# Kernel tuning notes

Measured on AMD Instinct MI355X. Metric: run time of the kernel, lower is better.

## Reference

```python
import jax, jax.numpy as jnp
import numpy as np

N, E, B = 10000, 20000, 400
ND, ED, D = 32, 16, 64


def setup_inputs() -> dict:
    key = jax.random.key(0)
    ks = jax.random.split(key, 32)

    def lin(k, out_d, in_d):
        kw, kb = jax.random.split(k)
        s = 1.0 / np.sqrt(in_d)
        return (jax.random.uniform(kw, (out_d, in_d), jnp.float32, -s, s),
                jax.random.uniform(kb, (out_d,), jnp.float32, -s, s))

    W_in, b_in = lin(ks[0], D, ND)
    W_e1, b_e1 = lin(ks[1], D, ED)
    W_e2, b_e2 = lin(ks[2], D * D, D)
    b_conv = jax.random.uniform(ks[3], (D,), jnp.float32, -1/8.0, 1/8.0)
    W_ih, b_ih = lin(ks[4], 3 * D, D)
    W_hh, b_hh = lin(ks[5], 3 * D, D)
    W_ih_l, b_ih_l = lin(ks[6], 4 * D, 2 * D)
    W_hh_l, b_hh_l = lin(ks[7], 4 * D, D)
    W_o1, b_o1 = lin(ks[8], D, 2 * D)
    W_o2, b_o2 = lin(ks[9], 1, D)

    x = jax.random.normal(ks[10], (N, ND), jnp.float32)
    edge_attr = jax.random.normal(ks[11], (E, ED), jnp.float32)
    edge_index = jax.random.randint(ks[12], (2, E), 0, N, jnp.int64)
    batch = jnp.sort(jax.random.randint(ks[13], (N,), 0, B, jnp.int64))

    return dict(x=x, edge_attr=edge_attr,
                W_in=W_in, b_in=b_in, W_e1=W_e1, b_e1=b_e1, W_e2=W_e2, b_e2=b_e2,
                b_conv=b_conv, W_ih=W_ih, b_ih=b_ih, W_hh=W_hh, b_hh=b_hh,
                W_ih_l=W_ih_l, b_ih_l=b_ih_l, W_hh_l=W_hh_l, b_hh_l=b_hh_l,
                W_o1=W_o1, b_o1=b_o1, W_o2=W_o2, b_o2=b_o2,
                edge_index=edge_index, batch=batch)


def reference(x, edge_attr, W_in, b_in, W_e1, b_e1, W_e2, b_e2, b_conv,
              W_ih, b_ih, W_hh, b_hh, W_ih_l, b_ih_l, W_hh_l, b_hh_l,
              W_o1, b_o1, W_o2, b_o2, edge_index, batch):
    src, dst = edge_index[0], edge_index[1]

    # in_linear
    out = jax.nn.relu(x @ W_in.T + b_in)            # [N, D]
    h = out                                          # GRU hidden (layer=1, seq=1)

    # edge-conditioned weights: MLP(edge_attr) -> [E, D, D]
    ew = (jax.nn.relu(edge_attr @ W_e1.T + b_e1) @ W_e2.T + b_e2).reshape(E, D, D)
    cnt = jnp.maximum(jax.ops.segment_sum(jnp.ones((E,), x.dtype), dst, N), 1.0)

    for _ in range(3):
        # NNConv: gather src nodes, per-edge matmul, scatter-mean to dst, + bias
        msg = jnp.einsum('ed,edf->ef', out[src], ew)                 # [E, D]
        agg = jax.ops.segment_sum(msg, dst, N) / cnt[:, None] + b_conv
        m = jax.nn.relu(agg)
        # GRU cell (torch gate order r, z, n)
        gi = m @ W_ih.T + b_ih
        gh = h @ W_hh.T + b_hh
        i_r, i_z, i_n = jnp.split(gi, 3, axis=-1)
        h_r, h_z, h_n = jnp.split(gh, 3, axis=-1)
        r = jax.nn.sigmoid(i_r + h_r)
        z = jax.nn.sigmoid(i_z + h_z)
        n = jnp.tanh(i_n + r * h_n)
        h = (1.0 - z) * n + z * h
        out = h

    # Set2Set pooling, processing_steps=3
    q_star = jnp.zeros((B, 2 * D), x.dtype)
    hl = jnp.zeros((B, D), x.dtype)
    cl = jnp.zeros((B, D), x.dtype)
    for _ in range(3):
        g = q_star @ W_ih_l.T + b_ih_l + hl @ W_hh_l.T + b_hh_l
        gi_, gf_, gg_, go_ = jnp.split(g, 4, axis=-1)   # torch order i,f,g,o
        cl = jax.nn.sigmoid(gf_) * cl + jax.nn.sigmoid(gi_) * jnp.tanh(gg_)
        hl = jax.nn.sigmoid(go_) * jnp.tanh(cl)
        q = hl                                           # [B, D]
        e = jnp.sum(out * q[batch], axis=-1)             # [N]
        mmax = jax.ops.segment_max(e, batch, B)
        a = jnp.exp(e - mmax[batch])
        a = a / jax.ops.segment_sum(a, batch, B)[batch]
        r_ = jax.ops.segment_sum(a[:, None] * out, batch, B)  # [B, D]
        q_star = jnp.concatenate([q, r_], axis=-1)

    o = jax.nn.relu(q_star @ W_o1.T + b_o1) @ W_o2.T + b_o2
    return o.reshape(-1)
```

## Files before the change

### kernel.cpp

```cpp
#include <hip/hip_runtime.h>
#include <math.h>


#define Nn 10000
#define Ee 20000
#define Bb 400
#define KSTEPS 130
#define S2S_CHUNK 1024

typedef __attribute__((ext_vector_type(8))) short bf16x8_t;
typedef __attribute__((ext_vector_type(4))) float f32x4_t;

__device__ __forceinline__ float sigmoidf_(float x) { return 1.f / (1.f + expf(-x)); }

__device__ __forceinline__ void split8(const float* p, bf16x8_t& Ahi_, bf16x8_t& Alo_) {
    union { bf16x8_t v; unsigned u[4]; } hi, lo;
#pragma unroll
    for (int ii = 0; ii < 4; ++ii) {
        float pa = p[2 * ii], pb = p[2 * ii + 1];
        unsigned ua = __float_as_uint(pa), ub = __float_as_uint(pb);
        hi.u[ii] = (ua >> 16) | (ub & 0xFFFF0000u);
        float la = pa - __uint_as_float(ua & 0xFFFF0000u);
        float lb = pb - __uint_as_float(ub & 0xFFFF0000u);
        lo.u[ii] = (__float_as_uint(la) >> 16) | (__float_as_uint(lb) & 0xFFFF0000u);
    }
    Ahi_ = hi.v; Alo_ = lo.v;
}

__global__ __launch_bounds__(256) void k_in_linear(const float* __restrict__ x,
                                                   const float* __restrict__ Win,
                                                   const float* __restrict__ bin,
                                                   float* __restrict__ out) {
    int idx = blockIdx.x * 256 + threadIdx.x;
    if (idx >= Nn * 64) return;
    int n = idx >> 6, j = idx & 63;
    const float* xr = x + n * 32;
    const float* w = Win + j * 32;
    float acc = bin[j];
#pragma unroll
    for (int k = 0; k < 32; ++k) acc += xr[k] * w[k];
    out[idx] = fmaxf(acc, 0.f);
}

__global__ __launch_bounds__(256) void k_edge_mlp1(const float* __restrict__ ea,
                                                   const float* __restrict__ W1,
                                                   const float* __restrict__ b1,
                                                   float* __restrict__ eh) {
    int idx = blockIdx.x * 256 + threadIdx.x;
    if (idx >= Ee * 64) return;
    int e = idx >> 6, j = idx & 63;
    const float* ar = ea + e * 16;
    const float* w = W1 + j * 16;
    float acc = b1[j];
#pragma unroll
    for (int k = 0; k < 16; ++k) acc += ar[k] * w[k];
    eh[idx] = fmaxf(acc, 0.f);
}

__global__ __launch_bounds__(256) void k_make_Bfat(const float* __restrict__ W2,
                                                   const float* __restrict__ b2,
                                                   unsigned short* __restrict__ Bfat) {
    int idx = blockIdx.x * 256 + threadIdx.x;
    if (idx >= KSTEPS * 4096) return;
    int i  = idx & 7;
    int l  = (idx >> 3) & 63;
    int nq = (idx >> 9) & 3;
    int h  = (idx >> 11) & 1;
    int ks = idx >> 12;
    int kap = ks * 32 + (l >> 4) * 8 + i;
    int f = nq * 16 + (l & 15);
    float w;
    if (kap < 4096) {
        int q = kap >> 6, d = kap & 63;
        w = W2[(size_t)(d * 64 + f) * 64 + q];
    } else {
        int d = kap - 4096;
        w = b2[d * 64 + f];
    }
    unsigned u = __float_as_uint(w);
    unsigned short outv;
    if (h == 0) {
        outv = (unsigned short)(u >> 16);
    } else {
        float lo = w - __uint_as_float(u & 0xFFFF0000u);
        outv = (unsigned short)(__float_as_uint(lo) >> 16);
    }
    Bfat[idx] = outv;
}

__global__ __launch_bounds__(256) void k_make_Wg(const float* __restrict__ Wih,
                                                 const float* __restrict__ Whh,
                                                 unsigned short* __restrict__ Wg) {
    int idx = blockIdx.x * 256 + threadIdx.x;
    if (idx >= 4 * 2 * 16 * 64 * 8) return;
    int i  = idx & 7;
    int l  = (idx >> 3) & 63;
    int t  = (idx >> 9) & 15;
    int h  = (idx >> 13) & 1;
    int ks = idx >> 14;
    int k = ks * 32 + (l >> 4) * 8 + i;
    int u = t * 16 + (l & 15);
    int j = u & 63, part = u >> 6;
    float w = 0.f;
    if (part == 0) w = (k < 64) ? Wih[(size_t)j * 64 + k]          : Whh[(size_t)j * 64 + (k - 64)];
    if (part == 1) w = (k < 64) ? Wih[(size_t)(64 + j) * 64 + k]   : Whh[(size_t)(64 + j) * 64 + (k - 64)];
    if (part == 2) w = (k < 64) ? Wih[(size_t)(128 + j) * 64 + k]  : 0.f;
    if (part == 3) w = (k < 64) ? 0.f : Whh[(size_t)(128 + j) * 64 + (k - 64)];
    unsigned uu = __float_as_uint(w);
    unsigned short outv;
    if (h == 0) {
        outv = (unsigned short)(uu >> 16);
    } else {
        float lo = w - __uint_as_float(uu & 0xFFFF0000u);
        outv = (unsigned short)(__float_as_uint(lo) >> 16);
    }
    Wg[idx] = outv;
}

__global__ __launch_bounds__(256, 3) void k_msg_mfma(const float* __restrict__ out,
                                                     const float* __restrict__ eh,
                                                     const unsigned short* __restrict__ Bfat,
                                                     const int* __restrict__ ei,
                                                     float* __restrict__ agg) {
    __shared__ float outs[128][64];
    __shared__ float ehs[128][20];
    __shared__ unsigned short Bst[4096];
    int tid = threadIdx.x;
    int ebase = blockIdx.x * 128;
    int ksplit = blockIdx.y;

    int ks0 = ksplit * 32 + (ksplit < 2 ? ksplit : 2);
    int ks1 = ks0 + (ksplit < 2 ? 33 : 32);
    int q0 = ks0 >> 1;
    int qn = ((min(ks1, 128) - 1) >> 1) - q0 + 1;

#pragma unroll
    for (int pass = 0; pass < 2; ++pass) {
        int el = pass * 64 + (tid >> 2), seg = tid & 3;
        int eg = ebase + el;
        bool v = eg < Ee;
        int s = v ? ei[eg] : 0;
        const float* orow = out + (size_t)s * 64 + seg * 16;
        float4 z = make_float4(0.f, 0.f, 0.f, 0.f);
#pragma unroll
        for (int c = 0; c < 4; ++c) {
            float4 ov = v ? *(const float4*)(orow + c * 4) : z;
            int f = (seg * 4 + c) ^ (el & 7);
            *(float4*)&outs[el][f * 4] = ov;
        }
        const float* erow = eh + (size_t)eg * 64;
        for (int j = seg; j < qn; j += 4)
            ehs[el][j] = v ? erow[q0 + j] : 0.f;
    }

    const float4* bsrc = (const float4*)(Bfat + (size_t)ks0 * 4096);
    float4 bpre0 = bsrc[tid];
    float4 bpre1 = bsrc[256 + tid];

    int lane = tid & 63;
    int wtile = tid >> 6;
    int m16 = lane & 15;
    int g = lane >> 4;
    int erA = wtile * 32 + m16;
    int erB = erA + 16;
    int eswA = erA & 7;
    int eswB = erB & 7;

    f32x4_t acc[2][4];
#pragma unroll
    for (int t = 0; t < 2; ++t)
#pragma unroll
        for (int nq = 0; nq < 4; ++nq) acc[t][nq] = (f32x4_t){0.f, 0.f, 0.f, 0.f};

    for (int ks = ks0; ks < ks1; ++ks) {
        *(float4*)&Bst[(size_t)tid * 8] = bpre0;
        *(float4*)&Bst[2048 + (size_t)tid * 8] = bpre1;
        __syncthreads();

        if (ks + 1 < ks1) {
            const float4* bn = (const float4*)(Bfat + (size_t)(ks + 1) * 4096);
            bpre0 = bn[tid];
            bpre1 = bn[256 + tid];
        }

        bf16x8_t bhi[4], blo[4];
#pragma unroll
        for (int nq = 0; nq < 4; ++nq) {
            bhi[nq] = *(const bf16x8_t*)&Bst[((size_t)nq * 64 + lane) * 8];
            blo[nq] = *(const bf16x8_t*)&Bst[((size_t)(4 + nq) * 64 + lane) * 8];
        }

        int fbase = (ks < 128) ? (ks & 1) * 8 + g * 2 : (ks - 128) * 8 + g * 2;

        {
            float ehq = (ks < 128) ? ehs[erA][(ks >> 1) - q0] : 1.f;
            float4 o1 = *(const float4*)&outs[erA][(fbase ^ eswA) * 4];
            float4 o2 = *(const float4*)&outs[erA][((fbase + 1) ^ eswA) * 4];
            float p[8] = {o1.x * ehq, o1.y * ehq, o1.z * ehq, o1.w * ehq,
                          o2.x * ehq, o2.y * ehq, o2.z * ehq, o2.w * ehq};
            bf16x8_t Ahi, Alo;
            split8(p, Ahi, Alo);
#pragma unroll
            for (int nq = 0; nq < 4; ++nq) {
                acc[0][nq] = __builtin_amdgcn_mfma_f32_16x16x32_bf16(Ahi, bhi[nq], acc[0][nq], 0, 0, 0);
                acc[0][nq] = __builtin_amdgcn_mfma_f32_16x16x32_bf16(Ahi, blo[nq], acc[0][nq], 0, 0, 0);
                acc[0][nq] = __builtin_amdgcn_mfma_f32_16x16x32_bf16(Alo, bhi[nq], acc[0][nq], 0, 0, 0);
            }
        }
        {
            float ehq = (ks < 128) ? ehs[erB][(ks >> 1) - q0] : 1.f;
            float4 o1 = *(const float4*)&outs[erB][(fbase ^ eswB) * 4];
            float4 o2 = *(const float4*)&outs[erB][((fbase + 1) ^ eswB) * 4];
            float p[8] = {o1.x * ehq, o1.y * ehq, o1.z * ehq, o1.w * ehq,
                          o2.x * ehq, o2.y * ehq, o2.z * ehq, o2.w * ehq};
            bf16x8_t Ahi, Alo;
            split8(p, Ahi, Alo);
#pragma unroll
            for (int nq = 0; nq < 4; ++nq) {
                acc[1][nq] = __builtin_amdgcn_mfma_f32_16x16x32_bf16(Ahi, bhi[nq], acc[1][nq], 0, 0, 0);
                acc[1][nq] = __builtin_amdgcn_mfma_f32_16x16x32_bf16(Ahi, blo[nq], acc[1][nq], 0, 0, 0);
                acc[1][nq] = __builtin_amdgcn_mfma_f32_16x16x32_bf16(Alo, bhi[nq], acc[1][nq], 0, 0, 0);
            }
        }
        __syncthreads();
    }

#pragma unroll
    for (int t = 0; t < 2; ++t) {
#pragma unroll
        for (int r = 0; r < 4; ++r) {
            int el = wtile * 32 + t * 16 + g * 4 + r;
            int eg = ebase + el;
            if (eg >= Ee) continue;
            int dn = ei[Ee + eg];
#pragma unroll
            for (int nq = 0; nq < 4; ++nq)
                atomicAdd(&agg[(size_t)dn * 64 + nq * 16 + m16], acc[t][nq][r]);
        }
    }
}

__global__ __launch_bounds__(256) void k_gru_mfma(const float* __restrict__ agg,
                                                  const float* __restrict__ cnt,
                                                  const float* __restrict__ bconv,
                                                  const unsigned short* __restrict__ Wg,
                                                  const float* __restrict__ bih,
                                                  const float* __restrict__ bhh,
                                                  float* __restrict__ out) {
    __shared__ float ms[64][68];
    __shared__ float hs[64][68];
    int tid = threadIdx.x;
    int nbase = blockIdx.x * 64;

    {
        int nl = tid >> 2, seg = tid & 3;
        int ng = nbase + nl;
        bool v = ng < Nn;
        float c = v ? cnt[ng] : 1.f;
        c = c < 1.f ? 1.f : c;
        float rc = 1.f / c;
        const float* arow = agg + (size_t)ng * 64 + seg * 16;
        const float* hrow = out + (size_t)ng * 64 + seg * 16;
#pragma unroll
        for (int c4 = 0; c4 < 4; ++c4) {
            int col = seg * 16 + c4 * 4;
            float4 z = make_float4(0.f, 0.f, 0.f, 0.f);
            float4 av = v ? *(const float4*)(arow + c4 * 4) : z;
            float4 hv = v ? *(const float4*)(hrow + c4 * 4) : z;
            ms[nl][col + 0] = fmaxf(av.x * rc + bconv[col + 0], 0.f);
            ms[nl][col + 1] = fmaxf(av.y * rc + bconv[col + 1], 0.f);
            ms[nl][col + 2] = fmaxf(av.z * rc + bconv[col + 2], 0.f);
            ms[nl][col + 3] = fmaxf(av.w * rc + bconv[col + 3], 0.f);
            *(float4*)&hs[nl][col] = hv;
        }
    }
    __syncthreads();

    int lane = tid & 63;
    int wtile = tid >> 6;
    int m16 = lane & 15;
    int g = lane >> 4;
    int er = wtile * 16 + m16;

    f32x4_t acc[16];
#pragma unroll
    for (int t = 0; t < 16; ++t) acc[t] = (f32x4_t){0.f, 0.f, 0.f, 0.f};

#pragma unroll
    for (int ks = 0; ks < 4; ++ks) {
        const float* src = (ks < 2) ? &ms[er][ks * 32 + g * 8]
                                    : &hs[er][(ks - 2) * 32 + g * 8];
        float p[8];
#pragma unroll
        for (int ii = 0; ii < 8; ++ii) p[ii] = src[ii];
        bf16x8_t Ahi, Alo;
        split8(p, Ahi, Alo);
        const unsigned short* bstep = Wg + (size_t)ks * (2 * 16 * 512);
#pragma unroll
        for (int t = 0; t < 16; ++t) {
            bf16x8_t bhi = *(const bf16x8_t*)(bstep + ((size_t)t * 64 + lane) * 8);
            bf16x8_t blo = *(const bf16x8_t*)(bstep + ((size_t)(16 + t) * 64 + lane) * 8);
            acc[t] = __builtin_amdgcn_mfma_f32_16x16x32_bf16(Ahi, bhi, acc[t], 0, 0, 0);
            acc[t] = __builtin_amdgcn_mfma_f32_16x16x32_bf16(Ahi, blo, acc[t], 0, 0, 0);
            acc[t] = __builtin_amdgcn_mfma_f32_16x16x32_bf16(Alo, bhi, acc[t], 0, 0, 0);
        }
    }

#pragma unroll
    for (int t2 = 0; t2 < 4; ++t2) {
        int jj = t2 * 16 + m16;
        float br = bih[jj] + bhh[jj];
        float bz = bih[64 + jj] + bhh[64 + jj];
        float bin_ = bih[128 + jj];
        float bhn = bhh[128 + jj];
#pragma unroll
        for (int r = 0; r < 4; ++r) {
            int nl2 = wtile * 16 + g * 4 + r;
            int ng2 = nbase + nl2;
            if (ng2 >= Nn) continue;
            float rg = sigmoidf_(acc[t2][r] + br);
            float z  = sigmoidf_(acc[4 + t2][r] + bz);
            float nn = tanhf(acc[8 + t2][r] + bin_ + rg * (acc[12 + t2][r] + bhn));
            float hv = hs[nl2][jj];
            out[(size_t)ng2 * 64 + jj] = (1.f - z) * nn + z * hv;
        }
    }
}

__global__ __launch_bounds__(256) void k_count_deg(const int* __restrict__ ei,
                                                   float* __restrict__ cnt) {
    int e = blockIdx.x * 256 + threadIdx.x;
    if (e >= Ee) return;
    atomicAdd(&cnt[ei[Ee + e]], 1.f);
}

__global__ __launch_bounds__(256) void k_count_batch(const int* __restrict__ batch,
                                                     int* __restrict__ bcount) {
    int n = blockIdx.x * 256 + threadIdx.x;
    if (n >= Nn) return;
    atomicAdd(&bcount[batch[n]], 1);
}

__global__ __launch_bounds__(64) void k_scan_batch(const int* __restrict__ bcount,
                                                   int* __restrict__ bstart) {
    int lane = threadIdx.x;
    const int PER = (Bb + 63) / 64;
    int base = lane * PER;
    int v[PER];
    int s = 0;
#pragma unroll
    for (int i = 0; i < PER; ++i) {
        int idx = base + i;
        int c = (idx < Bb) ? bcount[idx] : 0;
        v[i] = s;
        s += c;
    }
    int inc = s;
#pragma unroll
    for (int o = 1; o < 64; o <<= 1) {
        int t = __shfl_up(inc, o, 64);
        if (lane >= o) inc += t;
    }
    int excl = inc - s;
    int total = __shfl(inc, 63, 64);
#pragma unroll
    for (int i = 0; i < PER; ++i) {
        int idx = base + i;
        if (idx < Bb) bstart[idx] = excl + v[i];
    }
    if (lane == 63) bstart[Bb] = total;
}

__device__ __forceinline__ float block_reduce_max_(float v, float* red, int tid) {
#pragma unroll
    for (int o = 32; o; o >>= 1) v = fmaxf(v, __shfl_xor(v, o, 64));
    if ((tid & 63) == 0) red[tid >> 6] = v;
    __syncthreads();
    float r = fmaxf(fmaxf(red[0], red[1]), fmaxf(red[2], red[3]));
    __syncthreads();
    return r;
}
__device__ __forceinline__ float block_reduce_sum_(float v, float* red, int tid) {
#pragma unroll
    for (int o = 32; o; o >>= 1) v += __shfl_xor(v, o, 64);
    if ((tid & 63) == 0) red[tid >> 6] = v;
    __syncthreads();
    float r = (red[0] + red[1]) + (red[2] + red[3]);
    __syncthreads();
    return r;
}

__global__ __launch_bounds__(256) void k_set2set(const float* __restrict__ out,
                                                 const int* __restrict__ bstart,
                                                 const float* __restrict__ Wil,
                                                 const float* __restrict__ bil,
                                                 const float* __restrict__ Whl,
                                                 const float* __restrict__ bhl,
                                                 const float* __restrict__ Wo1,
                                                 const float* __restrict__ bo1,
                                                 const float* __restrict__ Wo2,
                                                 const float* __restrict__ bo2,
                                                 float* __restrict__ outp) {
    __shared__ float qs[128];
    __shared__ float hs2[64];
    __shared__ float cs[64];
    __shared__ float g_lds[256];
    __shared__ float e_lds[S2S_CHUNK];
    __shared__ float red[4];
    __shared__ float rpart[4][64];

    int b = blockIdx.x, tid = threadIdx.x;
    int lane = tid & 63, wv = tid >> 6;
    int s = bstart[b], eend = bstart[b + 1];
    int cntb = eend - s;

    if (tid < 128) qs[tid] = 0.f;
    if (tid < 64) { hs2[tid] = 0.f; cs[tid] = 0.f; }
    __syncthreads();

    for (int step = 0; step < 3; ++step) {
        {
            int u = tid;
            float acc = bil[u] + bhl[u];
            const float4* wi = (const float4*)(Wil + (size_t)u * 128);
#pragma unroll
            for (int k4 = 0; k4 < 32; ++k4) {
                float4 w = wi[k4];
                acc += qs[k4 * 4 + 0] * w.x + qs[k4 * 4 + 1] * w.y +
                       qs[k4 * 4 + 2] * w.z + qs[k4 * 4 + 3] * w.w;
            }
            const float4* wh = (const float4*)(Whl + (size_t)u * 64);
#pragma unroll
            for (int k4 = 0; k4 < 16; ++k4) {
                float4 w = wh[k4];
                acc += hs2[k4 * 4 + 0] * w.x + hs2[k4 * 4 + 1] * w.y +
                       hs2[k4 * 4 + 2] * w.z + hs2[k4 * 4 + 3] * w.w;
            }
            g_lds[u] = acc;
        }
        __syncthreads();
        if (tid < 64) {
            float c = sigmoidf_(g_lds[64 + tid]) * cs[tid] +
                      sigmoidf_(g_lds[tid]) * tanhf(g_lds[128 + tid]);
            cs[tid] = c;
            float h = sigmoidf_(g_lds[192 + tid]) * tanhf(c);
            hs2[tid] = h;
            qs[tid] = h;
        }
        __syncthreads();

        float gmax = -INFINITY, gsum = 0.f, racc = 0.f;
        for (int c0 = s; c0 < eend; c0 += S2S_CHUNK) {
            int clen = min(S2S_CHUNK, eend - c0);
            for (int i = tid; i < clen; i += 256) {
                const float4* orow = (const float4*)(out + (size_t)(c0 + i) * 64);
                float a0 = 0.f, a1 = 0.f, a2 = 0.f, a3 = 0.f;
#pragma unroll
                for (int k4 = 0; k4 < 16; k4 += 4) {
                    float4 o0 = orow[k4], o1 = orow[k4 + 1], o2 = orow[k4 + 2], o3 = orow[k4 + 3];
                    a0 += o0.x * qs[k4 * 4 + 0]  + o0.y * qs[k4 * 4 + 1]  + o0.z * qs[k4 * 4 + 2]  + o0.w * qs[k4 * 4 + 3];
                    a1 += o1.x * qs[k4 * 4 + 4]  + o1.y * qs[k4 * 4 + 5]  + o1.z * qs[k4 * 4 + 6]  + o1.w * qs[k4 * 4 + 7];
                    a2 += o2.x * qs[k4 * 4 + 8]  + o2.y * qs[k4 * 4 + 9]  + o2.z * qs[k4 * 4 + 10] + o2.w * qs[k4 * 4 + 11];
                    a3 += o3.x * qs[k4 * 4 + 12] + o3.y * qs[k4 * 4 + 13] + o3.z * qs[k4 * 4 + 14] + o3.w * qs[k4 * 4 + 15];
                }
                e_lds[i] = (a0 + a1) + (a2 + a3);
            }
            __syncthreads();
            float m = -INFINITY;
            for (int i = tid; i < clen; i += 256) m = fmaxf(m, e_lds[i]);
            float cmax = block_reduce_max_(m, red, tid);
            float nm = fmaxf(gmax, cmax);
            float scale = expf(gmax - nm);
            gsum *= scale; racc *= scale;
            float lsum = 0.f;
            for (int i = tid; i < clen; i += 256) {
                float av = expf(e_lds[i] - nm);
                e_lds[i] = av;
                lsum += av;
            }
            gsum += block_reduce_sum_(lsum, red, tid);
            for (int i = wv; i < clen; i += 4)
                racc += e_lds[i] * out[(size_t)(c0 + i) * 64 + lane];
            gmax = nm;
            __syncthreads();
        }
        rpart[wv][lane] = racc;
        __syncthreads();
        if (tid < 64) {
            float r = (rpart[0][tid] + rpart[1][tid]) + (rpart[2][tid] + rpart[3][tid]);
            qs[64 + tid] = (cntb > 0) ? r / gsum : 0.f;
        }
        __syncthreads();
    }

    if (tid < 64) {
        float acc = bo1[tid];
        const float4* w = (const float4*)(Wo1 + (size_t)tid * 128);
#pragma unroll
        for (int k4 = 0; k4 < 32; ++k4) {
            float4 wv4 = w[k4];
            acc += qs[k4 * 4 + 0] * wv4.x + qs[k4 * 4 + 1] * wv4.y +
                   qs[k4 * 4 + 2] * wv4.z + qs[k4 * 4 + 3] * wv4.w;
        }
        acc = fmaxf(acc, 0.f);
        float t = acc * Wo2[tid];
#pragma unroll
        for (int o = 32; o; o >>= 1) t += __shfl_xor(t, o, 64);
        if (tid == 0) outp[b] = t + bo2[0];
    }
}

extern "C" void kernel_launch(void* const* d_in, const int* in_sizes, int n_in,
                              void* d_out, int out_size, void* d_ws, size_t ws_size,
                              hipStream_t stream) {
    const float* x        = (const float*)d_in[0];
    const float* ea       = (const float*)d_in[1];
    const float* W_in     = (const float*)d_in[2];
    const float* b_in     = (const float*)d_in[3];
    const float* W_e1     = (const float*)d_in[4];
    const float* b_e1     = (const float*)d_in[5];
    const float* W_e2     = (const float*)d_in[6];
    const float* b_e2     = (const float*)d_in[7];
    const float* b_conv   = (const float*)d_in[8];
    const float* W_ih     = (const float*)d_in[9];
    const float* b_ih     = (const float*)d_in[10];
    const float* W_hh     = (const float*)d_in[11];
    const float* b_hh     = (const float*)d_in[12];
    const float* W_ih_l   = (const float*)d_in[13];
    const float* b_ih_l   = (const float*)d_in[14];
    const float* W_hh_l   = (const float*)d_in[15];
    const float* b_hh_l   = (const float*)d_in[16];
    const float* W_o1     = (const float*)d_in[17];
    const float* b_o1     = (const float*)d_in[18];
    const float* W_o2     = (const float*)d_in[19];
    const float* b_o2     = (const float*)d_in[20];
    const int*   ei       = (const int*)d_in[21];
    const int*   batch    = (const int*)d_in[22];
    float* outp = (float*)d_out;

    char* base = (char*)d_ws;
    size_t off = 0;
    auto carve = [&](size_t bytes) -> void* {
        void* p = base + off;
        off = (off + bytes + 255) & ~(size_t)255;
        return p;
    };
    float* out    = (float*)carve((size_t)Nn * 64 * 4);
    float* agg    = (float*)carve((size_t)Nn * 64 * 4);
    float* eh     = (float*)carve((size_t)Ee * 64 * 4);
    unsigned short* Bfat = (unsigned short*)carve((size_t)KSTEPS * 4096 * 2);
    unsigned short* Wg   = (unsigned short*)carve((size_t)4 * 2 * 16 * 64 * 8 * 2);
    float* cnt    = (float*)carve((size_t)Nn * 4);
    int*   bcount = (int*)carve((size_t)Bb * 4);
    int*   bstart = (int*)carve((size_t)(Bb + 1) * 4);
    if (off > ws_size) return;

    hipMemsetAsync(cnt, 0, (size_t)Nn * 4, stream);
    hipMemsetAsync(bcount, 0, (size_t)Bb * 4, stream);

    k_in_linear<<<(Nn * 64) / 256, 256, 0, stream>>>(x, W_in, b_in, out);
    k_edge_mlp1<<<(Ee * 64) / 256, 256, 0, stream>>>(ea, W_e1, b_e1, eh);
    k_make_Bfat<<<(KSTEPS * 4096) / 256, 256, 0, stream>>>(W_e2, b_e2, Bfat);
    k_make_Wg<<<(4 * 2 * 16 * 64 * 8) / 256, 256, 0, stream>>>(W_ih, W_hh, Wg);
    k_count_deg<<<(Ee + 255) / 256, 256, 0, stream>>>(ei, cnt);
    k_count_batch<<<(Nn + 255) / 256, 256, 0, stream>>>(batch, bcount);
    k_scan_batch<<<1, 64, 0, stream>>>(bcount, bstart);

    int eblocks = (Ee + 127) / 128;
    int nblocks = (Nn + 63) / 64;
    for (int it = 0; it < 3; ++it) {
        hipMemsetAsync(agg, 0, (size_t)Nn * 64 * 4, stream);
        k_msg_mfma<<<dim3(eblocks, 4), 256, 0, stream>>>(out, eh, Bfat, ei, agg);
        k_gru_mfma<<<nblocks, 256, 0, stream>>>(agg, cnt, b_conv, Wg, b_ih, b_hh, out);
    }

    k_set2set<<<Bb, 256, 0, stream>>>(out, bstart, W_ih_l, b_ih_l, W_hh_l, b_hh_l,
                                      W_o1, b_o1, W_o2, b_o2, outp);
}
```

Before: 335.9 us.

## Keep gathered rows in registers and read B fragments directly from global

```diff
diff --git a/kernel.cpp b/kernel.cpp
--- a/kernel.cpp
+++ b/kernel.cpp
@@ -122,9 +122,9 @@
                                                      const unsigned short* __restrict__ Bfat,
                                                      const int* __restrict__ ei,
                                                      float* __restrict__ agg) {
-    __shared__ float outs[128][64];
     __shared__ float ehs[128][20];
-    __shared__ unsigned short Bst[4096];
+    __shared__ int srcs[128];
+    __shared__ int dsts[128];
     int tid = threadIdx.x;
     int ebase = blockIdx.x * 128;
     int ksplit = blockIdx.y;
@@ -134,28 +134,19 @@
     int q0 = ks0 >> 1;
     int qn = ((min(ks1, 128) - 1) >> 1) - q0 + 1;
 
-#pragma unroll
-    for (int pass = 0; pass < 2; ++pass) {
-        int el = pass * 64 + (tid >> 2), seg = tid & 3;
+    {
+        int el = tid >> 1, seg = tid & 1;
         int eg = ebase + el;
         bool v = eg < Ee;
-        int s = v ? ei[eg] : 0;
-        const float* orow = out + (size_t)s * 64 + seg * 16;
-        float4 z = make_float4(0.f, 0.f, 0.f, 0.f);
-#pragma unroll
-        for (int c = 0; c < 4; ++c) {
-            float4 ov = v ? *(const float4*)(orow + c * 4) : z;
-            int f = (seg * 4 + c) ^ (el & 7);
-            *(float4*)&outs[el][f * 4] = ov;
+        if (seg == 0) {
+            srcs[el] = v ? ei[eg] : 0;
+            dsts[el] = v ? ei[Ee + eg] : 0;
         }
         const float* erow = eh + (size_t)eg * 64;
-        for (int j = seg; j < qn; j += 4)
+        for (int j = seg; j < qn; j += 2)
             ehs[el][j] = v ? erow[q0 + j] : 0.f;
     }
-
-    const float4* bsrc = (const float4*)(Bfat + (size_t)ks0 * 4096);
-    float4 bpre0 = bsrc[tid];
-    float4 bpre1 = bsrc[256 + tid];
+    __syncthreads();
 
     int lane = tid & 63;
     int wtile = tid >> 6;
@@ -163,8 +154,25 @@
     int g = lane >> 4;
     int erA = wtile * 32 + m16;
     int erB = erA + 16;
-    int eswA = erA & 7;
-    int eswB = erB & 7;
+
+    float a0[2][8], a1[2][8];
+    {
+        const float* rA = out + (size_t)srcs[erA] * 64;
+        const float* rB = out + (size_t)srcs[erB] * 64;
+        float4 v0, v1;
+        v0 = *(const float4*)(rA + g * 8);      v1 = *(const float4*)(rA + g * 8 + 4);
+        a0[0][0]=v0.x; a0[0][1]=v0.y; a0[0][2]=v0.z; a0[0][3]=v0.w;
+        a0[0][4]=v1.x; a0[0][5]=v1.y; a0[0][6]=v1.z; a0[0][7]=v1.w;
+        v0 = *(const float4*)(rA + 32 + g * 8); v1 = *(const float4*)(rA + 36 + g * 8);
+        a1[0][0]=v0.x; a1[0][1]=v0.y; a1[0][2]=v0.z; a1[0][3]=v0.w;
+        a1[0][4]=v1.x; a1[0][5]=v1.y; a1[0][6]=v1.z; a1[0][7]=v1.w;
+        v0 = *(const float4*)(rB + g * 8);      v1 = *(const float4*)(rB + g * 8 + 4);
+        a0[1][0]=v0.x; a0[1][1]=v0.y; a0[1][2]=v0.z; a0[1][3]=v0.w;
+        a0[1][4]=v1.x; a0[1][5]=v1.y; a0[1][6]=v1.z; a0[1][7]=v1.w;
+        v0 = *(const float4*)(rB + 32 + g * 8); v1 = *(const float4*)(rB + 36 + g * 8);
+        a1[1][0]=v0.x; a1[1][1]=v0.y; a1[1][2]=v0.z; a1[1][3]=v0.w;
+        a1[1][4]=v1.x; a1[1][5]=v1.y; a1[1][6]=v1.z; a1[1][7]=v1.w;
+    }
 
     f32x4_t acc[2][4];
 #pragma unroll
@@ -172,57 +180,40 @@
 #pragma unroll
         for (int nq = 0; nq < 4; ++nq) acc[t][nq] = (f32x4_t){0.f, 0.f, 0.f, 0.f};
 
-    for (int ks = ks0; ks < ks1; ++ks) {
-        *(float4*)&Bst[(size_t)tid * 8] = bpre0;
-        *(float4*)&Bst[2048 + (size_t)tid * 8] = bpre1;
-        __syncthreads();
-
-        if (ks + 1 < ks1) {
-            const float4* bn = (const float4*)(Bfat + (size_t)(ks + 1) * 4096);
-            bpre0 = bn[tid];
-            bpre1 = bn[256 + tid];
-        }
-
+    auto body = [&](int ks, const float (&Av)[2][8], float qA, float qB) {
+        const unsigned short* bstep = Bfat + (size_t)ks * 4096;
         bf16x8_t bhi[4], blo[4];
 #pragma unroll
         for (int nq = 0; nq < 4; ++nq) {
-            bhi[nq] = *(const bf16x8_t*)&Bst[((size_t)nq * 64 + lane) * 8];
-            blo[nq] = *(const bf16x8_t*)&Bst[((size_t)(4 + nq) * 64 + lane) * 8];
-        }
-
-        int fbase = (ks < 128) ? (ks & 1) * 8 + g * 2 : (ks - 128) * 8 + g * 2;
-
-        {
-            float ehq = (ks < 128) ? ehs[erA][(ks >> 1) - q0] : 1.f;
-            float4 o1 = *(const float4*)&outs[erA][(fbase ^ eswA) * 4];
-            float4 o2 = *(const float4*)&outs[erA][((fbase + 1) ^ eswA) * 4];
-            float p[8] = {o1.x * ehq, o1.y * ehq, o1.z * ehq, o1.w * ehq,
-                          o2.x * ehq, o2.y * ehq, o2.z * ehq, o2.w * ehq};
-            bf16x8_t Ahi, Alo;
-            split8(p, Ahi, Alo);
-#pragma unroll
-            for (int nq = 0; nq < 4; ++nq) {
-                acc[0][nq] = __builtin_amdgcn_mfma_f32_16x16x32_bf16(Ahi, bhi[nq], acc[0][nq], 0, 0, 0);
-                acc[0][nq] = __builtin_amdgcn_mfma_f32_16x16x32_bf16(Ahi, blo[nq], acc[0][nq], 0, 0, 0);
-                acc[0][nq] = __builtin_amdgcn_mfma_f32_16x16x32_bf16(Alo, bhi[nq], acc[0][nq], 0, 0, 0);
-            }
-        }
-        {
-            float ehq = (ks < 128) ? ehs[erB][(ks >> 1) - q0] : 1.f;
-            float4 o1 = *(const float4*)&outs[erB][(fbase ^ eswB) * 4];
-            float4 o2 = *(const float4*)&outs[erB][((fbase + 1) ^ eswB) * 4];
-            float p[8] = {o1.x * ehq, o1.y * ehq, o1.z * ehq, o1.w * ehq,
-                          o2.x * ehq, o2.y * ehq, o2.z * ehq, o2.w * ehq};
-            bf16x8_t Ahi, Alo;
-            split8(p, Ahi, Alo);
-#pragma unroll
-            for (int nq = 0; nq < 4; ++nq) {
-                acc[1][nq] = __builtin_amdgcn_mfma_f32_16x16x32_bf16(Ahi, bhi[nq], acc[1][nq], 0, 0, 0);
-                acc[1][nq] = __builtin_amdgcn_mfma_f32_16x16x32_bf16(Ahi, blo[nq], acc[1][nq], 0, 0, 0);
-                acc[1][nq] = __builtin_amdgcn_mfma_f32_16x16x32_bf16(Alo, bhi[nq], acc[1][nq], 0, 0, 0);
-            }
-        }
-        __syncthreads();
+            bhi[nq] = *(const bf16x8_t*)(bstep + ((size_t)(nq * 64 + lane)) * 8);
+            blo[nq] = *(const bf16x8_t*)(bstep + ((size_t)((4 + nq) * 64 + lane)) * 8);
+        }
+        float pA[8], pB[8];
+#pragma unroll
+        for (int i = 0; i < 8; ++i) { pA[i] = Av[0][i] * qA; pB[i] = Av[1][i] * qB; }
+        bf16x8_t AhiA, AloA, AhiB, AloB;
+        split8(pA, AhiA, AloA);
+        split8(pB, AhiB, AloB);
+#pragma unroll
+        for (int nq = 0; nq < 4; ++nq) {
+            acc[0][nq] = __builtin_amdgcn_mfma_f32_16x16x32_bf16(AhiA, bhi[nq], acc[0][nq], 0, 0, 0);
+            acc[0][nq] = __builtin_amdgcn_mfma_f32_16x16x32_bf16(AhiA, blo[nq], acc[0][nq], 0, 0, 0);
+            acc[0][nq] = __builtin_amdgcn_mfma_f32_16x16x32_bf16(AloA, bhi[nq], acc[0][nq], 0, 0, 0);
+            acc[1][nq] = __builtin_amdgcn_mfma_f32_16x16x32_bf16(AhiB, bhi[nq], acc[1][nq], 0, 0, 0);
+            acc[1][nq] = __builtin_amdgcn_mfma_f32_16x16x32_bf16(AhiB, blo[nq], acc[1][nq], 0, 0, 0);
+            acc[1][nq] = __builtin_amdgcn_mfma_f32_16x16x32_bf16(AloB, bhi[nq], acc[1][nq], 0, 0, 0);
+        }
+    };
+
+    for (int kp = ks0 & ~1; kp < ks1; kp += 2) {
+        float qA = 1.f, qB = 1.f;
+        if (kp < 128) {
+            int qi = (kp >> 1) - q0;
+            qA = ehs[erA][qi];
+            qB = ehs[erB][qi];
+        }
+        if (kp >= ks0)    body(kp,     a0, qA, qB);
+        if (kp + 1 < ks1) body(kp + 1, a1, qA, qB);
     }
 
 #pragma unroll
@@ -232,7 +223,7 @@
             int el = wtile * 32 + t * 16 + g * 4 + r;
             int eg = ebase + el;
             if (eg >= Ee) continue;
-            int dn = ei[Ee + eg];
+            int dn = dsts[el];
 #pragma unroll
             for (int nq = 0; nq < 4; ++nq)
                 atomicAdd(&agg[(size_t)dn * 64 + nq * 16 + m16], acc[t][nq][r]);
```

Result: no change. 332.9 us (-0.9%).
